# Kernel optimization log

Measured on AMD Instinct MI355X. Metric: run time of the kernel, lower is better.

## Reference

```python
import jax, jax.numpy as jnp
import numpy as np
from jax import lax

FIR_TAPS = np.array([1.0, 3.0, 3.0, 1.0], dtype=np.float32)
FACTOR = 2
GAIN = 1.0


def _fir_kernel(C):
    # _setup_kernel: outer product, normalize to sum 1; upsample scales by gain*factor**2
    k = np.outer(FIR_TAPS, FIR_TAPS)
    k = k / k.sum() * (GAIN * FACTOR ** 2)  # 4x4 kernel, sum == 4
    k = jnp.asarray(k, jnp.float32)
    return jnp.tile(k[None, None], (C, 1, 1, 1))  # [C,1,4,4] depthwise


def setup_inputs() -> dict:
    key = jax.random.key(0)
    k1, k2, k3 = jax.random.split(key, 3)
    x = jax.random.normal(k1, (16, 256, 64, 64), jnp.float32)
    W = jax.random.normal(k2, (256, 256, 3, 3), jnp.float32) * 0.02
    b = jax.random.normal(k3, (256,), jnp.float32) * 0.02
    return {"x": x, "W": W, "b": b}


def reference(x, W, b):
    B, C, H, Wd = x.shape
    kern = _fir_kernel(C)
    # upfirdn2d upsample: zero-insert by 2 (lhs_dilation), pad0=2 / pad1=1(+up-1=2),
    # depthwise FIR correlation -> [B, C, 2H, 2W]
    p0, p1 = 2, 2  # pad1 = p//2 + (factor-1) trailing zeros folded into padding
    h = lax.conv_general_dilated(
        x, kern, window_strides=(1, 1), padding=((p0, p1), (p0, p1)),
        lhs_dilation=(FACTOR, FACTOR),
        dimension_numbers=("NCHW", "OIHW", "NCHW"), feature_group_count=C)
    # 3x3 conv, padding=1, stride=1 -> [B, out_ch, 2H, 2W]
    y = lax.conv_general_dilated(
        h, W, window_strides=(1, 1), padding=((1, 1), (1, 1)),
        dimension_numbers=("NCHW", "OIHW", "NCHW"))
    return y + b[None, :, None, None]
```

## Files before the change

### kernel.cpp

```cpp
#include <hip/hip_runtime.h>
#include <hip/hip_bf16.h>
#include <stdint.h>

typedef __attribute__((ext_vector_type(8))) short bf16x8;
typedef __attribute__((ext_vector_type(4))) float f32x4;

#define PH 130
#define NT 36

__device__ __forceinline__ short f2bf(float f) {
  uint32_t u = __builtin_bit_cast(uint32_t, f);
  u = (u + 0x7FFFu + ((u >> 16) & 1u)) >> 16;
  return (short)u;
}

__device__ __forceinline__ uint32_t pack2bf(float lo, float hi) {
  return ((uint32_t)(uint16_t)f2bf(hi) << 16) | (uint16_t)f2bf(lo);
}

__device__ __forceinline__ void gload16(const void* g, void* l) {
  __builtin_amdgcn_global_load_lds(
      (const __attribute__((address_space(1))) void*)g,
      (__attribute__((address_space(3))) void*)l, 16, 0, 0);
}

__global__ void wpack(const float* __restrict__ W, short* __restrict__ A) {
  int tid = blockIdx.x * 256 + threadIdx.x;
  if (tid >= 256 * 2304) return;
  int co = tid / 2304;
  int r  = tid - co * 2304;
  int tap = r >> 8, ci = r & 255;
  A[tid] = f2bf(W[((size_t)(co * 256 + ci)) * 9 + tap]);
}

__global__ void fir_up(const float* __restrict__ x, short* __restrict__ hT) {
  const int bt = blockIdx.x;
  const int b = bt / 65, t = bt - b * 65;
  const int ci0 = blockIdx.y << 6;
  const int tid = threadIdx.x;

  if (t == 64) {
    short* r0 = hT + ((size_t)(b * PH + 0) * PH) * 256 + ci0;
    short* r1 = hT + ((size_t)(b * PH + 129) * PH) * 256 + ci0;
    for (int idx = tid; idx < PH * 32; idx += 256) {
      int qp = idx >> 5, c2 = (idx & 31) * 2;
      *(uint32_t*)&r0[(size_t)qp * 256 + c2] = 0u;
      *(uint32_t*)&r1[(size_t)qp * 256 + c2] = 0u;
    }
    return;
  }

  __shared__ float F[2][64][65];
#pragma unroll
  for (int it = 0; it < 4; ++it) {
    int idx = it * 256 + tid;
    int ci = idx >> 4, jq = idx & 15;
    const float* base = &x[((size_t)(b * 256 + ci0 + ci) * 64) * 64 + jq * 4];
    f32x4 vm = {0.f, 0.f, 0.f, 0.f}, vp = {0.f, 0.f, 0.f, 0.f};
    f32x4 v0 = *(const f32x4*)(base + (size_t)t * 64);
    if (t >= 1)  vm = *(const f32x4*)(base + (size_t)(t - 1) * 64);
    if (t <= 62) vp = *(const f32x4*)(base + (size_t)(t + 1) * 64);
#pragma unroll
    for (int e = 0; e < 4; ++e) {
      F[0][jq * 4 + e][ci] = 0.25f * vm[e] + 0.75f * v0[e];
      F[1][jq * 4 + e][ci] = 0.75f * v0[e] + 0.25f * vp[e];
    }
  }
  __syncthreads();

  const int c2 = (tid & 31) * 2;
  const int qg = tid >> 5;
#pragma unroll
  for (int r = 0; r < 2; ++r) {
    short* outrow = hT + ((size_t)(b * PH + (2 * t + 1 + r)) * PH) * 256 + ci0;
    for (int qp = qg; qp < PH; qp += 8) {
      uint32_t out = 0u;
      if (qp >= 1 && qp <= 128) {
        int q = qp - 1;
        int par = q & 1;
        int jb = (q >> 1) - 1 + par;
        float wc0 = par ? 0.75f : 0.25f;
        float wc1 = par ? 0.25f : 0.75f;
        float v00 = 0.f, v01 = 0.f, v10 = 0.f, v11 = 0.f;
        if (jb >= 0)     { v00 = F[r][jb][c2];     v01 = F[r][jb][c2 + 1]; }
        if (jb + 1 < 64) { v10 = F[r][jb + 1][c2]; v11 = F[r][jb + 1][c2 + 1]; }
        out = pack2bf(wc0 * v00 + wc1 * v10, wc0 * v01 + wc1 * v11);
      }
      *(uint32_t*)&outrow[(size_t)qp * 256 + c2] = out;
    }
  }
}

__global__ __launch_bounds__(512, 4) void conv3x3_gemm(
    const short* __restrict__ hT, const short* __restrict__ Wp,
    const float* __restrict__ bias, float* __restrict__ y) {
  __shared__ short ldsA[3][8192];
  __shared__ short ldsB[2][8192];
  const int tid = threadIdx.x;
  const int lane = tid & 63, w = tid >> 6;
  const int wm = w >> 2, wn = w & 3;

  const int bid = blockIdx.x;
  const int tau = (bid & 7) * 512 + (bid >> 3);
  const int mt = tau >> 1, nh = tau & 1;
  const int b = mt >> 7, p = mt & 127;

  const short* srcA[2];
  const short* srcB[2];
#pragma unroll
  for (int i = 0; i < 2; ++i) {
    int o = i * 8192 + w * 1024 + lane * 16;
    int L = o ^ (((o >> 7) & 7) << 4);
    int row = L >> 7, kk = (L & 127) >> 1;
    srcA[i] = hT + ((size_t)((b * PH + p) * PH + row)) * 256 + kk;
    srcB[i] = Wp + (size_t)(nh * 128 + row) * 2304 + kk;
  }

  auto offA = [&](int t) {
    int tap = t >> 2, ci0 = (t & 3) << 6;
    int dm = (tap >= 6) ? 2 : (tap >= 3) ? 1 : 0;
    int dn = tap - 3 * dm;
    return (dm * PH + dn) * 256 + ci0;
  };
  auto offB = [&](int t) { return (t >> 2) * 256 + ((t & 3) << 6); };

  auto stageA = [&](int t) {
    int o = offA(t);
    short* dst = &ldsA[t % 3][0];
#pragma unroll
    for (int i = 0; i < 2; ++i)
      gload16(srcA[i] + o, dst + i * 4096 + w * 512);
  };
  auto stageB = [&](int t) {
    int o = offB(t);
    short* dst = &ldsB[t & 1][0];
#pragma unroll
    for (int i = 0; i < 2; ++i)
      gload16(srcB[i] + o, dst + i * 4096 + w * 512);
  };

  int aP[2], bP[2];
#pragma unroll
  for (int ks = 0; ks < 2; ++ks) {
    int La = (wm * 64 + (lane & 15)) * 128 + (lane >> 4) * 16 + ks * 64;
    aP[ks] = La ^ ((lane & 7) << 4);
    int Lb = (wn * 32 + (lane & 15)) * 128 + (lane >> 4) * 16 + ks * 64;
    bP[ks] = Lb ^ ((lane & 7) << 4);
  }

  f32x4 acc[4][2];
#pragma unroll
  for (int m = 0; m < 4; ++m)
#pragma unroll
    for (int n = 0; n < 2; ++n) acc[m][n] = (f32x4){0.f, 0.f, 0.f, 0.f};

  stageA(0); stageB(0); stageA(1);
  asm volatile("s_waitcnt vmcnt(2)" ::: "memory");
  __builtin_amdgcn_s_barrier();

  for (int t = 0; t < NT; ++t) {
    const char* LA = (const char*)&ldsA[t % 3][0];
    const char* LB = (const char*)&ldsB[t & 1][0];

    bf16x8 a_[2][4], b_[2][2];
#pragma unroll
    for (int ks = 0; ks < 2; ++ks) {
#pragma unroll
      for (int m = 0; m < 4; ++m) a_[ks][m] = *(const bf16x8*)(LA + aP[ks] + m * 2048);
#pragma unroll
      for (int n = 0; n < 2; ++n) b_[ks][n] = *(const bf16x8*)(LB + bP[ks] + n * 2048);
    }
    if (t + 1 < NT) stageB(t + 1);
    if (t + 2 < NT) stageA(t + 2);
    asm volatile("s_waitcnt lgkmcnt(0)" ::: "memory");
    __builtin_amdgcn_s_setprio(1);
#pragma unroll
    for (int m = 0; m < 4; ++m)
#pragma unroll
      for (int n = 0; n < 2; ++n) {
        acc[m][n] = __builtin_amdgcn_mfma_f32_16x16x32_bf16(a_[0][m], b_[0][n], acc[m][n], 0, 0, 0);
        acc[m][n] = __builtin_amdgcn_mfma_f32_16x16x32_bf16(a_[1][m], b_[1][n], acc[m][n], 0, 0, 0);
      }
    __builtin_amdgcn_s_setprio(0);
    if (t < NT - 2)       asm volatile("s_waitcnt vmcnt(2)" ::: "memory");
    else if (t == NT - 2) asm volatile("s_waitcnt vmcnt(0)" ::: "memory");
    __builtin_amdgcn_s_barrier();
  }

#pragma unroll
  for (int n = 0; n < 2; ++n) {
    int co = nh * 128 + wn * 32 + n * 16 + (lane & 15);
    float bv = bias[co];
    float* yp = y + (((size_t)(b * 256 + co)) * 128 + p) * 128;
#pragma unroll
    for (int m = 0; m < 4; ++m) {
      int q0 = wm * 64 + m * 16 + ((lane >> 4) << 2);
      f32x4 vv = acc[m][n];
      vv[0] += bv; vv[1] += bv; vv[2] += bv; vv[3] += bv;
      *(f32x4*)(yp + q0) = vv;
    }
  }
}

extern "C" void kernel_launch(void* const* d_in, const int* in_sizes, int n_in,
                              void* d_out, int out_size, void* d_ws, size_t ws_size,
                              hipStream_t stream) {
  const float* x    = (const float*)d_in[0];
  const float* W    = (const float*)d_in[1];
  const float* bias = (const float*)d_in[2];
  float* y = (float*)d_out;

  const size_t hT_bytes = (size_t)16 * PH * PH * 256 * 2;
  const size_t A_bytes  = (size_t)256 * 2304 * 2;
  if (ws_size < hT_bytes + A_bytes) return;

  short* hT = (short*)d_ws;
  short* Wp = (short*)((char*)d_ws + hT_bytes);

  wpack<<<(256 * 2304 + 255) / 256, 256, 0, stream>>>(W, Wp);
  dim3 g1(16 * 65, 4);
  fir_up<<<g1, 256, 0, stream>>>(x, hT);
  conv3x3_gemm<<<4096, 512, 0, stream>>>(hT, Wp, bias, y);
}
```

Baseline: 375.7 us.

## Halve GEMM K-step and use 4 waves with 64x64 warp tiles

Restructures the conv3x3 implicit GEMM from 8 waves each holding a 64x32 sub-tile with K=64 per step to 4 waves each holding a 64x64 sub-tile with K=32 per step. The iteration count doubles, A and B now share a single triple-buffered pipeline, and the LDS swizzle is adapted to 64-byte rows. Larger per-wave tiles improve register-level reuse and halve LDS use per block so more blocks can be resident. In exchange, barriers per output tile double and each wave needs more accumulator registers.

```diff
diff --git a/kernel.cpp b/kernel.cpp
--- a/kernel.cpp
+++ b/kernel.cpp
@@ -6,7 +6,7 @@
 typedef __attribute__((ext_vector_type(4))) float f32x4;
 
 #define PH 130
-#define NT 36
+#define NT 72
 
 __device__ __forceinline__ short f2bf(float f) {
   uint32_t u = __builtin_bit_cast(uint32_t, f);
@@ -91,14 +91,14 @@
   }
 }
 
-__global__ __launch_bounds__(512, 4) void conv3x3_gemm(
+__global__ __launch_bounds__(256, 3) void conv3x3_gemm(
     const short* __restrict__ hT, const short* __restrict__ Wp,
     const float* __restrict__ bias, float* __restrict__ y) {
-  __shared__ short ldsA[3][8192];
-  __shared__ short ldsB[2][8192];
+  __shared__ short ldsA[3][4096];
+  __shared__ short ldsB[3][4096];
   const int tid = threadIdx.x;
   const int lane = tid & 63, w = tid >> 6;
-  const int wm = w >> 2, wn = w & 3;
+  const int wm = w >> 1, wn = w & 1;
 
   const int bid = blockIdx.x;
   const int tau = (bid & 7) * 512 + (bid >> 3);
@@ -109,87 +109,72 @@
   const short* srcB[2];
 #pragma unroll
   for (int i = 0; i < 2; ++i) {
-    int o = i * 8192 + w * 1024 + lane * 16;
-    int L = o ^ (((o >> 7) & 7) << 4);
-    int row = L >> 7, kk = (L & 127) >> 1;
+    int o = i * 4096 + tid * 16;
+    int L = o ^ (((o >> 7) & 3) << 4);
+    int row = L >> 6, kk = (L & 63) >> 1;
     srcA[i] = hT + ((size_t)((b * PH + p) * PH + row)) * 256 + kk;
     srcB[i] = Wp + (size_t)(nh * 128 + row) * 2304 + kk;
   }
 
   auto offA = [&](int t) {
-    int tap = t >> 2, ci0 = (t & 3) << 6;
+    int tap = t >> 3, ci0 = (t & 7) << 5;
     int dm = (tap >= 6) ? 2 : (tap >= 3) ? 1 : 0;
     int dn = tap - 3 * dm;
     return (dm * PH + dn) * 256 + ci0;
   };
-  auto offB = [&](int t) { return (t >> 2) * 256 + ((t & 3) << 6); };
-
-  auto stageA = [&](int t) {
-    int o = offA(t);
-    short* dst = &ldsA[t % 3][0];
-#pragma unroll
-    for (int i = 0; i < 2; ++i)
-      gload16(srcA[i] + o, dst + i * 4096 + w * 512);
+  auto offB = [&](int t) { return (t >> 3) * 256 + ((t & 7) << 5); };
+
+  auto stage = [&](int t) {
+    int buf = t % 3;
+    int oa = offA(t), ob = offB(t);
+#pragma unroll
+    for (int i = 0; i < 2; ++i) {
+      gload16(srcA[i] + oa, &ldsA[buf][i * 2048] + (tid << 3));
+      gload16(srcB[i] + ob, &ldsB[buf][i * 2048] + (tid << 3));
+    }
   };
-  auto stageB = [&](int t) {
-    int o = offB(t);
-    short* dst = &ldsB[t & 1][0];
-#pragma unroll
-    for (int i = 0; i < 2; ++i)
-      gload16(srcB[i] + o, dst + i * 4096 + w * 512);
-  };
-
-  int aP[2], bP[2];
-#pragma unroll
-  for (int ks = 0; ks < 2; ++ks) {
-    int La = (wm * 64 + (lane & 15)) * 128 + (lane >> 4) * 16 + ks * 64;
-    aP[ks] = La ^ ((lane & 7) << 4);
-    int Lb = (wn * 32 + (lane & 15)) * 128 + (lane >> 4) * 16 + ks * 64;
-    bP[ks] = Lb ^ ((lane & 7) << 4);
-  }
-
-  f32x4 acc[4][2];
+
+  const int aP = ((wm * 64 + (lane & 15)) * 64 + (lane >> 4) * 16)
+                 ^ ((((lane & 15) >> 1) & 3) << 4);
+  const int bP = ((wn * 64 + (lane & 15)) * 64 + (lane >> 4) * 16)
+                 ^ ((((lane & 15) >> 1) & 3) << 4);
+
+  f32x4 acc[4][4];
 #pragma unroll
   for (int m = 0; m < 4; ++m)
 #pragma unroll
-    for (int n = 0; n < 2; ++n) acc[m][n] = (f32x4){0.f, 0.f, 0.f, 0.f};
-
-  stageA(0); stageB(0); stageA(1);
-  asm volatile("s_waitcnt vmcnt(2)" ::: "memory");
+    for (int n = 0; n < 4; ++n) acc[m][n] = (f32x4){0.f, 0.f, 0.f, 0.f};
+
+  stage(0); stage(1);
+  asm volatile("s_waitcnt vmcnt(4)" ::: "memory");
   __builtin_amdgcn_s_barrier();
 
   for (int t = 0; t < NT; ++t) {
     const char* LA = (const char*)&ldsA[t % 3][0];
-    const char* LB = (const char*)&ldsB[t & 1][0];
-
-    bf16x8 a_[2][4], b_[2][2];
-#pragma unroll
-    for (int ks = 0; ks < 2; ++ks) {
-#pragma unroll
-      for (int m = 0; m < 4; ++m) a_[ks][m] = *(const bf16x8*)(LA + aP[ks] + m * 2048);
-#pragma unroll
-      for (int n = 0; n < 2; ++n) b_[ks][n] = *(const bf16x8*)(LB + bP[ks] + n * 2048);
-    }
-    if (t + 1 < NT) stageB(t + 1);
-    if (t + 2 < NT) stageA(t + 2);
+    const char* LB = (const char*)&ldsB[t % 3][0];
+
+    bf16x8 a_[4], b_[4];
+#pragma unroll
+    for (int m = 0; m < 4; ++m) a_[m] = *(const bf16x8*)(LA + aP + m * 1024);
+#pragma unroll
+    for (int n = 0; n < 4; ++n) b_[n] = *(const bf16x8*)(LB + bP + n * 1024);
+    if (t + 2 < NT) stage(t + 2);
     asm volatile("s_waitcnt lgkmcnt(0)" ::: "memory");
     __builtin_amdgcn_s_setprio(1);
 #pragma unroll
     for (int m = 0; m < 4; ++m)
 #pragma unroll
-      for (int n = 0; n < 2; ++n) {
-        acc[m][n] = __builtin_amdgcn_mfma_f32_16x16x32_bf16(a_[0][m], b_[0][n], acc[m][n], 0, 0, 0);
-        acc[m][n] = __builtin_amdgcn_mfma_f32_16x16x32_bf16(a_[1][m], b_[1][n], acc[m][n], 0, 0, 0);
-      }
+      for (int n = 0; n < 4; ++n)
+        acc[m][n] = __builtin_amdgcn_mfma_f32_16x16x32_bf16(a_[m], b_[n], acc[m][n], 0, 0, 0);
     __builtin_amdgcn_s_setprio(0);
-    if (t < NT - 2)       asm volatile("s_waitcnt vmcnt(2)" ::: "memory");
+    if (t < NT - 2)       asm volatile("s_waitcnt vmcnt(4)" ::: "memory");
     else if (t == NT - 2) asm volatile("s_waitcnt vmcnt(0)" ::: "memory");
-    __builtin_amdgcn_s_barrier();
-  }
-
-#pragma unroll
-  for (int n = 0; n < 2; ++n) {
-    int co = nh * 128 + wn * 32 + n * 16 + (lane & 15);
+    if (t < NT - 1) __builtin_amdgcn_s_barrier();
+  }
+
+#pragma unroll
+  for (int n = 0; n < 4; ++n) {
+    int co = nh * 128 + wn * 64 + n * 16 + (lane & 15);
     float bv = bias[co];
     float* yp = y + (((size_t)(b * 256 + co)) * 128 + p) * 128;
 #pragma unroll
@@ -220,5 +205,5 @@
   wpack<<<(256 * 2304 + 255) / 256, 256, 0, stream>>>(W, Wp);
   dim3 g1(16 * 65, 4);
   fir_up<<<g1, 256, 0, stream>>>(x, hT);
-  conv3x3_gemm<<<4096, 512, 0, stream>>>(hT, Wp, bias, y);
-}
+  conv3x3_gemm<<<4096, 256, 0, stream>>>(hT, Wp, bias, y);
+}
```

Result: slower. 444.8 us (+18.4%).
